# Performance work log

Hardware: AMD Instinct MI355X
Metric: run time of the kernel (lower is better)

## Reference

```python
import jax, jax.numpy as jnp
import numpy as np

TOKENS, HIDDEN, N_EXPERTS = 16384, 2048, 64
JITTER_EPS = 0.01
Z_LOSS_COEFF = 0.001


def setup_inputs() -> dict:
    key = jax.random.key(0)
    k1, k2 = jax.random.split(key)
    x = jax.random.normal(k1, (TOKENS, HIDDEN), dtype=jnp.float32)
    w = jax.random.normal(k2, (N_EXPERTS, HIDDEN), dtype=jnp.float32) * 0.02  # router weight [E,H]
    return {"x": x, "w": w}


def _route_pass(scores_sel, scores, jitter_eps):
    # scores_sel: logits possibly with -inf at already-selected expert (top-2 pass)
    # scores:     original logits (used for abs/clamp factor, as in torch code)
    mx = jnp.max(scores_sel, axis=-1, keepdims=True)                      # [N,1]
    factor = jnp.maximum(jnp.abs(scores), mx)                             # scores.abs().clamp(min=mx)
    mask = jax.lax.stop_gradient((mx - scores) / factor > 2.0 * jitter_eps)
    masked_logits = jnp.where(mask, -jnp.inf, scores_sel)
    # eval path (training=False): selected_experts = argmax of (masked-for-selection) scores
    sel = jnp.argmax(scores_sel, axis=-1)[..., None]                      # [N,1] int
    gates = jax.nn.softmax(masked_logits, axis=-1)
    # mask_for_one: selected == argmax(gates) holds deterministically in eval -> 1.0
    mult = jnp.take_along_axis(gates, sel, axis=-1)                       # [N,1]
    return mult, sel


def reference(x, w):
    logits = x @ w.T                                                      # [N,E]
    # z-loss (identity on logits in forward; scalar returned for completeness)
    z_loss = Z_LOSS_COEFF * jnp.mean(jnp.square(jax.nn.logsumexp(logits, axis=-1)))
    original_gates = jax.nn.softmax(logits, axis=-1)
    # top-1 pass
    m1, s1 = _route_pass(logits, logits, JITTER_EPS)
    # top-2 pass: mask out the first selection
    e_idx = jnp.arange(logits.shape[-1])[None, :]
    scores2 = jnp.where(e_idx == s1, -jnp.inf, logits)
    m2, s2 = _route_pass(scores2, logits, JITTER_EPS)
    multiplier = jnp.concatenate([m1, m2], axis=-1)                       # [N,2]
    selected_experts = jnp.concatenate([s1, s2], axis=-1)                 # [N,2]
    return multiplier, original_gates, selected_experts, z_loss
```

## Files before the change

### kernel.cpp

```cpp
#include <hip/hip_runtime.h>
#include <math.h>

#define TOKENS 16384
#define HIDDEN 2048
#define NEXP   64
#define MT     32
#define NBLK   (TOKENS / MT)

#define GATES_OFF (TOKENS * 2)
#define SEL_OFF   (GATES_OFF + TOKENS * NEXP)
#define Z_OFF     (SEL_OFF + TOKENS * 2)

#define WIMG_BYTES (NEXP * HIDDEN * 2 * 2)

typedef __attribute__((ext_vector_type(8))) _Float16 f16x8;
typedef __attribute__((ext_vector_type(4))) float    f32x4;

__device__ __forceinline__ float wave_sum64(float v) {
    #pragma unroll
    for (int s = 1; s < 64; s <<= 1) v += __shfl_xor(v, s, 64);
    return v;
}

__global__ __launch_bounds__(256) void wconvert(
    const float* __restrict__ w, uint4* __restrict__ wimg)
{
    const int s = blockIdx.x * 256 + threadIdx.x;
    const int c    = s >> 10;
    const int r    = s & 1023;
    const int l    = r & 63;
    const int nt   = (r >> 6) & 1;
    const int kh   = (r >> 7) & 1;
    const int term = (r >> 8) & 1;
    const int eh   = (r >> 9) & 1;
    const int e = eh * 32 + nt * 16 + (l & 15);
    const int k = c * 64 + kh * 32 + (l >> 4) * 8;

    const float* src = w + (size_t)e * HIDDEN + k;
    union { _Float16 f[8]; uint4 u; } o;
    #pragma unroll
    for (int j = 0; j < 8; ++j) {
        const float v = src[j];
        const _Float16 h = (_Float16)v;
        o.f[j] = (term == 0) ? h : (_Float16)((v - (float)h) * 4096.f);
    }
    wimg[s] = o.u;
}

__device__ __forceinline__ void cvt_split(const float4 a, const float4 b,
                                          f16x8& hi, f16x8& lo) {
    union { _Float16 f[8]; f16x8 v; } H, L;
    #pragma unroll
    for (int j = 0; j < 4; ++j) {
        const float s0 = (&a.x)[j];
        const float s1 = (&b.x)[j];
        const _Float16 h0 = (_Float16)s0;
        const _Float16 h1 = (_Float16)s1;
        H.f[j]     = h0;
        H.f[j + 4] = h1;
        L.f[j]     = (_Float16)((s0 - (float)h0) * 4096.f);
        L.f[j + 4] = (_Float16)((s1 - (float)h1) * 4096.f);
    }
    hi = H.v; lo = L.v;
}

struct Pipe {
    float4 ra0, ra1, ra2, ra3;
    f16x8  bh[4], bl[4];
};

__device__ __forceinline__ void loadA(Pipe& P, const float* ax0,
                                      const float* ax1, int s) {
    P.ra0 = *(const float4*)(ax0 + s * 32);
    P.ra1 = *(const float4*)(ax0 + s * 32 + 4);
    P.ra2 = *(const float4*)(ax1 + s * 32);
    P.ra3 = *(const float4*)(ax1 + s * 32 + 4);
}

__device__ __forceinline__ void loadB(Pipe& P, const uint4* wB, int s) {
    const uint4* p = wB + (s >> 1) * 1024 + (s & 1) * 128;
    P.bh[0] = *(const f16x8*)(p);
    P.bh[1] = *(const f16x8*)(p + 64);
    P.bh[2] = *(const f16x8*)(p + 512);
    P.bh[3] = *(const f16x8*)(p + 576);
    P.bl[0] = *(const f16x8*)(p + 256);
    P.bl[1] = *(const f16x8*)(p + 320);
    P.bl[2] = *(const f16x8*)(p + 768);
    P.bl[3] = *(const f16x8*)(p + 832);
}

__device__ __forceinline__ void domfma(const Pipe& P,
                                       const f16x8 Ah0, const f16x8 Ah1,
                                       const f16x8 Al0, const f16x8 Al1,
                                       f32x4 (&acc0)[2][4], f32x4 (&acc1)[2][4]) {
    #pragma unroll
    for (int g = 0; g < 4; ++g) {
        acc0[0][g] = __builtin_amdgcn_mfma_f32_16x16x32_f16(Ah0, P.bh[g], acc0[0][g], 0, 0, 0);
        acc1[0][g] = __builtin_amdgcn_mfma_f32_16x16x32_f16(Ah0, P.bl[g], acc1[0][g], 0, 0, 0);
        acc1[0][g] = __builtin_amdgcn_mfma_f32_16x16x32_f16(Al0, P.bh[g], acc1[0][g], 0, 0, 0);
        acc0[1][g] = __builtin_amdgcn_mfma_f32_16x16x32_f16(Ah1, P.bh[g], acc0[1][g], 0, 0, 0);
        acc1[1][g] = __builtin_amdgcn_mfma_f32_16x16x32_f16(Ah1, P.bl[g], acc1[1][g], 0, 0, 0);
        acc1[1][g] = __builtin_amdgcn_mfma_f32_16x16x32_f16(Al1, P.bh[g], acc1[1][g], 0, 0, 0);
    }
}

__global__ __launch_bounds__(256, 2) void router_main(
    const float* __restrict__ x, const uint4* __restrict__ wimg,
    float* __restrict__ out, float* __restrict__ zpartial)
{
    __shared__ __align__(16) float lg[4][32 * 66];
    __shared__ float zred[4];

    const int tid  = threadIdx.x;
    const int wv   = __builtin_amdgcn_readfirstlane(tid >> 6);
    const int lane = tid & 63;
    const int t0   = blockIdx.x * MT;

    const float* ax0 = x + (size_t)(t0 + (lane & 15)) * HIDDEN
                         + wv * 512 + (lane >> 4) * 8;
    const float* ax1 = ax0 + 16 * HIDDEN;

    const uint4* wB = wimg + wv * 8192 + lane;

    f32x4 acc0[2][4], acc1[2][4];
    #pragma unroll
    for (int mt = 0; mt < 2; ++mt)
        #pragma unroll
        for (int g = 0; g < 4; ++g) { acc0[mt][g] = (f32x4)0.f; acc1[mt][g] = (f32x4)0.f; }

    Pipe PA, PB;
    f16x8 Ah0, Ah1, Al0, Al1;

    loadA(PA, ax0, ax1, 0); loadB(PA, wB, 0);
    loadA(PB, ax0, ax1, 1); loadB(PB, wB, 1);

    #pragma unroll
    for (int s = 0; s < 16; s += 2) {
        cvt_split(PA.ra0, PA.ra1, Ah0, Al0);
        cvt_split(PA.ra2, PA.ra3, Ah1, Al1);
        if (s + 2 < 16) loadA(PA, ax0, ax1, s + 2);
        domfma(PA, Ah0, Ah1, Al0, Al1, acc0, acc1);
        if (s + 2 < 16) loadB(PA, wB, s + 2);

        cvt_split(PB.ra0, PB.ra1, Ah0, Al0);
        cvt_split(PB.ra2, PB.ra3, Ah1, Al1);
        if (s + 3 < 16) loadA(PB, ax0, ax1, s + 3);
        domfma(PB, Ah0, Ah1, Al0, Al1, acc0, acc1);
        if (s + 3 < 16) loadB(PB, wB, s + 3);
    }

    #pragma unroll
    for (int mt = 0; mt < 2; ++mt)
        #pragma unroll
        for (int g = 0; g < 4; ++g)
            #pragma unroll
            for (int r = 0; r < 4; ++r) {
                const int tok = mt * 16 + (lane >> 4) * 4 + r;
                const int e   = (g >> 1) * 32 + (g & 1) * 16 + (lane & 15);
                lg[wv][tok * 66 + e] = acc0[mt][g][r] + acc1[mt][g][r] * (1.f / 4096.f);
            }
    __syncthreads();

    float zsum = 0.f;
    for (int tt = 0; tt < 8; ++tt) {
        const int t = wv * 8 + tt;
        const int li = t * 66 + lane;
        const float v = lg[0][li] + lg[1][li] + lg[2][li] + lg[3][li];

        float bv = v; int bi = lane;
        #pragma unroll
        for (int s = 1; s < 64; s <<= 1) {
            const float ov = __shfl_xor(bv, s, 64);
            const int   oi = __shfl_xor(bi, s, 64);
            if (ov > bv || (ov == bv && oi < bi)) { bv = ov; bi = oi; }
        }
        const float max1 = bv; const int s1 = bi;

        const float e1 = expf(v - max1);
        const float sume = wave_sum64(e1);
        out[GATES_OFF + (size_t)(t0 + t) * NEXP + lane] = e1 / sume;
        const float lse = max1 + logf(sume);
        zsum += lse * lse;

        const bool mask1 = (max1 - v) > 0.02f * fmaxf(fabsf(v), max1);
        const float sum1 = wave_sum64(mask1 ? 0.f : e1);

        float bv2 = (lane == s1) ? -INFINITY : v; int bi2 = lane;
        #pragma unroll
        for (int s = 1; s < 64; s <<= 1) {
            const float ov = __shfl_xor(bv2, s, 64);
            const int   oi = __shfl_xor(bi2, s, 64);
            if (ov > bv2 || (ov == bv2 && oi < bi2)) { bv2 = ov; bi2 = oi; }
        }
        const float max2 = bv2; const int s2 = bi2;

        const bool mask2 = (max2 - v) > 0.02f * fmaxf(fabsf(v), max2);
        const float p2v = (mask2 || lane == s1) ? 0.f : expf(v - max2);
        const float sum2 = wave_sum64(p2v);

        if (lane == 0) {
            const size_t trow = (size_t)(t0 + t) * 2;
            out[trow + 0] = 1.f / sum1;
            out[trow + 1] = 1.f / sum2;
            out[SEL_OFF + trow + 0] = (float)s1;
            out[SEL_OFF + trow + 1] = (float)s2;
        }
    }

    if (lane == 0) zred[wv] = zsum;
    __syncthreads();
    if (tid == 0)
        zpartial[blockIdx.x] = zred[0] + zred[1] + zred[2] + zred[3];
}

__global__ __launch_bounds__(256) void zfinal(
    const float* __restrict__ zpartial, float* __restrict__ out)
{
    const int tid = threadIdx.x;
    float v = zpartial[tid] + zpartial[tid + 256];
    v = wave_sum64(v);
    __shared__ float red[4];
    if ((tid & 63) == 0) red[tid >> 6] = v;
    __syncthreads();
    if (tid == 0) {
        const float tot = red[0] + red[1] + red[2] + red[3];
        out[Z_OFF] = 0.001f * (tot / (float)TOKENS);
    }
}

extern "C" void kernel_launch(void* const* d_in, const int* in_sizes, int n_in,
                              void* d_out, int out_size, void* d_ws, size_t ws_size,
                              hipStream_t stream) {
    const float* x = (const float*)d_in[0];
    const float* w = (const float*)d_in[1];
    float* out = (float*)d_out;

    uint4* wimg     = (uint4*)d_ws;
    float* zpartial = (float*)((char*)d_ws + WIMG_BYTES);

    wconvert<<<128, 256, 0, stream>>>(w, wimg);
    router_main<<<NBLK, 256, 0, stream>>>(x, wimg, out, zpartial);
    zfinal<<<1, 256, 0, stream>>>(zpartial, out);
}
```

Baseline: 218.1 us.

## Fuse weight conversion and z-loss reduction into single router kernel

```diff
diff --git a/kernel.cpp b/kernel.cpp
--- a/kernel.cpp
+++ b/kernel.cpp
@@ -11,40 +11,16 @@
 #define SEL_OFF   (GATES_OFF + TOKENS * NEXP)
 #define Z_OFF     (SEL_OFF + TOKENS * 2)
 
-#define WIMG_BYTES (NEXP * HIDDEN * 2 * 2)
-
 typedef __attribute__((ext_vector_type(8))) _Float16 f16x8;
 typedef __attribute__((ext_vector_type(4))) float    f32x4;
 
+__device__ float    g_zacc = 0.f;
+__device__ unsigned g_cnt  = 0u;
+
 __device__ __forceinline__ float wave_sum64(float v) {
     #pragma unroll
     for (int s = 1; s < 64; s <<= 1) v += __shfl_xor(v, s, 64);
     return v;
-}
-
-__global__ __launch_bounds__(256) void wconvert(
-    const float* __restrict__ w, uint4* __restrict__ wimg)
-{
-    const int s = blockIdx.x * 256 + threadIdx.x;
-    const int c    = s >> 10;
-    const int r    = s & 1023;
-    const int l    = r & 63;
-    const int nt   = (r >> 6) & 1;
-    const int kh   = (r >> 7) & 1;
-    const int term = (r >> 8) & 1;
-    const int eh   = (r >> 9) & 1;
-    const int e = eh * 32 + nt * 16 + (l & 15);
-    const int k = c * 64 + kh * 32 + (l >> 4) * 8;
-
-    const float* src = w + (size_t)e * HIDDEN + k;
-    union { _Float16 f[8]; uint4 u; } o;
-    #pragma unroll
-    for (int j = 0; j < 8; ++j) {
-        const float v = src[j];
-        const _Float16 h = (_Float16)v;
-        o.f[j] = (term == 0) ? h : (_Float16)((v - (float)h) * 4096.f);
-    }
-    wimg[s] = o.u;
 }
 
 __device__ __forceinline__ void cvt_split(const float4 a, const float4 b,
@@ -64,49 +40,50 @@
     hi = H.v; lo = L.v;
 }
 
-struct Pipe {
-    float4 ra0, ra1, ra2, ra3;
-    f16x8  bh[4], bl[4];
-};
-
-__device__ __forceinline__ void loadA(Pipe& P, const float* ax0,
-                                      const float* ax1, int s) {
-    P.ra0 = *(const float4*)(ax0 + s * 32);
-    P.ra1 = *(const float4*)(ax0 + s * 32 + 4);
-    P.ra2 = *(const float4*)(ax1 + s * 32);
-    P.ra3 = *(const float4*)(ax1 + s * 32 + 4);
-}
-
-__device__ __forceinline__ void loadB(Pipe& P, const uint4* wB, int s) {
-    const uint4* p = wB + (s >> 1) * 1024 + (s & 1) * 128;
-    P.bh[0] = *(const f16x8*)(p);
-    P.bh[1] = *(const f16x8*)(p + 64);
-    P.bh[2] = *(const f16x8*)(p + 512);
-    P.bh[3] = *(const f16x8*)(p + 576);
-    P.bl[0] = *(const f16x8*)(p + 256);
-    P.bl[1] = *(const f16x8*)(p + 320);
-    P.bl[2] = *(const f16x8*)(p + 768);
-    P.bl[3] = *(const f16x8*)(p + 832);
-}
-
-__device__ __forceinline__ void domfma(const Pipe& P,
-                                       const f16x8 Ah0, const f16x8 Ah1,
-                                       const f16x8 Al0, const f16x8 Al1,
-                                       f32x4 (&acc0)[2][4], f32x4 (&acc1)[2][4]) {
+struct Stage { float4 a[4]; float4 b[8]; };
+
+__device__ __forceinline__ void load_stage(
+    Stage& S, const float* ax0, const float* ax1,
+    const float* bw0, const float* bw1, const float* bw2, const float* bw3,
+    int s)
+{
+    const int o = s * 32;
+    S.a[0] = *(const float4*)(ax0 + o);
+    S.a[1] = *(const float4*)(ax0 + o + 4);
+    S.a[2] = *(const float4*)(ax1 + o);
+    S.a[3] = *(const float4*)(ax1 + o + 4);
+    S.b[0] = *(const float4*)(bw0 + o);
+    S.b[1] = *(const float4*)(bw0 + o + 4);
+    S.b[2] = *(const float4*)(bw1 + o);
+    S.b[3] = *(const float4*)(bw1 + o + 4);
+    S.b[4] = *(const float4*)(bw2 + o);
+    S.b[5] = *(const float4*)(bw2 + o + 4);
+    S.b[6] = *(const float4*)(bw3 + o);
+    S.b[7] = *(const float4*)(bw3 + o + 4);
+}
+
+__device__ __forceinline__ void consume_stage(
+    const Stage& S, f32x4 (&acc0)[2][4], f32x4 (&acc1)[2][4])
+{
+    f16x8 Ah0, Al0, Ah1, Al1;
+    cvt_split(S.a[0], S.a[1], Ah0, Al0);
+    cvt_split(S.a[2], S.a[3], Ah1, Al1);
     #pragma unroll
     for (int g = 0; g < 4; ++g) {
-        acc0[0][g] = __builtin_amdgcn_mfma_f32_16x16x32_f16(Ah0, P.bh[g], acc0[0][g], 0, 0, 0);
-        acc1[0][g] = __builtin_amdgcn_mfma_f32_16x16x32_f16(Ah0, P.bl[g], acc1[0][g], 0, 0, 0);
-        acc1[0][g] = __builtin_amdgcn_mfma_f32_16x16x32_f16(Al0, P.bh[g], acc1[0][g], 0, 0, 0);
-        acc0[1][g] = __builtin_amdgcn_mfma_f32_16x16x32_f16(Ah1, P.bh[g], acc0[1][g], 0, 0, 0);
-        acc1[1][g] = __builtin_amdgcn_mfma_f32_16x16x32_f16(Ah1, P.bl[g], acc1[1][g], 0, 0, 0);
-        acc1[1][g] = __builtin_amdgcn_mfma_f32_16x16x32_f16(Al1, P.bh[g], acc1[1][g], 0, 0, 0);
-    }
-}
-
-__global__ __launch_bounds__(256, 2) void router_main(
-    const float* __restrict__ x, const uint4* __restrict__ wimg,
-    float* __restrict__ out, float* __restrict__ zpartial)
+        f16x8 bh, bl;
+        cvt_split(S.b[2 * g], S.b[2 * g + 1], bh, bl);
+        acc0[0][g] = __builtin_amdgcn_mfma_f32_16x16x32_f16(Ah0, bh, acc0[0][g], 0, 0, 0);
+        acc0[1][g] = __builtin_amdgcn_mfma_f32_16x16x32_f16(Ah1, bh, acc0[1][g], 0, 0, 0);
+        acc1[0][g] = __builtin_amdgcn_mfma_f32_16x16x32_f16(Ah0, bl, acc1[0][g], 0, 0, 0);
+        acc1[0][g] = __builtin_amdgcn_mfma_f32_16x16x32_f16(Al0, bh, acc1[0][g], 0, 0, 0);
+        acc1[1][g] = __builtin_amdgcn_mfma_f32_16x16x32_f16(Ah1, bl, acc1[1][g], 0, 0, 0);
+        acc1[1][g] = __builtin_amdgcn_mfma_f32_16x16x32_f16(Al1, bh, acc1[1][g], 0, 0, 0);
+    }
+}
+
+__global__ __launch_bounds__(256, 2) void router_full(
+    const float* __restrict__ x, const float* __restrict__ w,
+    float* __restrict__ out)
 {
     __shared__ __align__(16) float lg[4][32 * 66];
     __shared__ float zred[4];
@@ -116,11 +93,15 @@
     const int lane = tid & 63;
     const int t0   = blockIdx.x * MT;
 
-    const float* ax0 = x + (size_t)(t0 + (lane & 15)) * HIDDEN
-                         + wv * 512 + (lane >> 4) * 8;
+    const int kbase = wv * 512 + (lane >> 4) * 8;
+
+    const float* ax0 = x + (size_t)(t0 + (lane & 15)) * HIDDEN + kbase;
     const float* ax1 = ax0 + 16 * HIDDEN;
 
-    const uint4* wB = wimg + wv * 8192 + lane;
+    const float* bw0 = w + (size_t)(lane & 15) * HIDDEN + kbase;
+    const float* bw1 = bw0 + 16 * HIDDEN;
+    const float* bw2 = bw0 + 32 * HIDDEN;
+    const float* bw3 = bw0 + 48 * HIDDEN;
 
     f32x4 acc0[2][4], acc1[2][4];
     #pragma unroll
@@ -128,25 +109,17 @@
         #pragma unroll
         for (int g = 0; g < 4; ++g) { acc0[mt][g] = (f32x4)0.f; acc1[mt][g] = (f32x4)0.f; }
 
-    Pipe PA, PB;
-    f16x8 Ah0, Ah1, Al0, Al1;
-
-    loadA(PA, ax0, ax1, 0); loadB(PA, wB, 0);
-    loadA(PB, ax0, ax1, 1); loadB(PB, wB, 1);
+    Stage SA, SB;
+
+    load_stage(SA, ax0, ax1, bw0, bw1, bw2, bw3, 0);
+    load_stage(SB, ax0, ax1, bw0, bw1, bw2, bw3, 1);
 
     #pragma unroll
     for (int s = 0; s < 16; s += 2) {
-        cvt_split(PA.ra0, PA.ra1, Ah0, Al0);
-        cvt_split(PA.ra2, PA.ra3, Ah1, Al1);
-        if (s + 2 < 16) loadA(PA, ax0, ax1, s + 2);
-        domfma(PA, Ah0, Ah1, Al0, Al1, acc0, acc1);
-        if (s + 2 < 16) loadB(PA, wB, s + 2);
-
-        cvt_split(PB.ra0, PB.ra1, Ah0, Al0);
-        cvt_split(PB.ra2, PB.ra3, Ah1, Al1);
-        if (s + 3 < 16) loadA(PB, ax0, ax1, s + 3);
-        domfma(PB, Ah0, Ah1, Al0, Al1, acc0, acc1);
-        if (s + 3 < 16) loadB(PB, wB, s + 3);
+        consume_stage(SA, acc0, acc1);
+        if (s + 2 < 16) load_stage(SA, ax0, ax1, bw0, bw1, bw2, bw3, s + 2);
+        consume_stage(SB, acc0, acc1);
+        if (s + 3 < 16) load_stage(SB, ax0, ax1, bw0, bw1, bw2, bw3, s + 3);
     }
 
     #pragma unroll
@@ -156,7 +129,7 @@
             #pragma unroll
             for (int r = 0; r < 4; ++r) {
                 const int tok = mt * 16 + (lane >> 4) * 4 + r;
-                const int e   = (g >> 1) * 32 + (g & 1) * 16 + (lane & 15);
+                const int e   = g * 16 + (lane & 15);
                 lg[wv][tok * 66 + e] = acc0[mt][g][r] + acc1[mt][g][r] * (1.f / 4096.f);
             }
     __syncthreads();
@@ -209,22 +182,18 @@
 
     if (lane == 0) zred[wv] = zsum;
     __syncthreads();
-    if (tid == 0)
-        zpartial[blockIdx.x] = zred[0] + zred[1] + zred[2] + zred[3];
-}
-
-__global__ __launch_bounds__(256) void zfinal(
-    const float* __restrict__ zpartial, float* __restrict__ out)
-{
-    const int tid = threadIdx.x;
-    float v = zpartial[tid] + zpartial[tid + 256];
-    v = wave_sum64(v);
-    __shared__ float red[4];
-    if ((tid & 63) == 0) red[tid >> 6] = v;
-    __syncthreads();
+
     if (tid == 0) {
-        const float tot = red[0] + red[1] + red[2] + red[3];
-        out[Z_OFF] = 0.001f * (tot / (float)TOKENS);
+        const float bz = zred[0] + zred[1] + zred[2] + zred[3];
+        atomicAdd(&g_zacc, bz);
+        __threadfence();
+        const unsigned old = atomicAdd(&g_cnt, 1u);
+        if (old == NBLK - 1) {
+            __threadfence();
+            const float tot = atomicExch(&g_zacc, 0.f);
+            atomicExch(&g_cnt, 0u);
+            out[Z_OFF] = 0.001f * (tot / (float)TOKENS);
+        }
     }
 }
 
@@ -234,11 +203,7 @@
     const float* x = (const float*)d_in[0];
     const float* w = (const float*)d_in[1];
     float* out = (float*)d_out;
-
-    uint4* wimg     = (uint4*)d_ws;
-    float* zpartial = (float*)((char*)d_ws + WIMG_BYTES);
-
-    wconvert<<<128, 256, 0, stream>>>(w, wimg);
-    router_main<<<NBLK, 256, 0, stream>>>(x, wimg, out, zpartial);
-    zfinal<<<1, 256, 0, stream>>>(zpartial, out);
-}
+    (void)d_ws; (void)ws_size;
+
+    router_full<<<NBLK, 256, 0, stream>>>(x, w, out);
+}
```

Measured after the change: 238.6 us. 1.09x slower.

## Halve token tile per block, raise occupancy, fuse z-loss reduction via atomics

Applied to the files above, without the earlier changes.

```diff
diff --git a/kernel.cpp b/kernel.cpp
--- a/kernel.cpp
+++ b/kernel.cpp
@@ -4,7 +4,7 @@
 #define TOKENS 16384
 #define HIDDEN 2048
 #define NEXP   64
-#define MT     32
+#define MT     16
 #define NBLK   (TOKENS / MT)
 
 #define GATES_OFF (TOKENS * 2)
@@ -15,6 +15,9 @@
 
 typedef __attribute__((ext_vector_type(8))) _Float16 f16x8;
 typedef __attribute__((ext_vector_type(4))) float    f32x4;
+
+__device__ float    g_zacc = 0.f;
+__device__ unsigned g_cnt  = 0u;
 
 __device__ __forceinline__ float wave_sum64(float v) {
     #pragma unroll
@@ -64,51 +67,44 @@
     hi = H.v; lo = L.v;
 }
 
-struct Pipe {
-    float4 ra0, ra1, ra2, ra3;
+struct Stage {
+    float4 a0, a1;
     f16x8  bh[4], bl[4];
 };
 
-__device__ __forceinline__ void loadA(Pipe& P, const float* ax0,
-                                      const float* ax1, int s) {
-    P.ra0 = *(const float4*)(ax0 + s * 32);
-    P.ra1 = *(const float4*)(ax0 + s * 32 + 4);
-    P.ra2 = *(const float4*)(ax1 + s * 32);
-    P.ra3 = *(const float4*)(ax1 + s * 32 + 4);
-}
-
-__device__ __forceinline__ void loadB(Pipe& P, const uint4* wB, int s) {
+__device__ __forceinline__ void load_stage(Stage& S, const float* ax0,
+                                           const uint4* wB, int s) {
+    S.a0 = *(const float4*)(ax0 + s * 32);
+    S.a1 = *(const float4*)(ax0 + s * 32 + 4);
     const uint4* p = wB + (s >> 1) * 1024 + (s & 1) * 128;
-    P.bh[0] = *(const f16x8*)(p);
-    P.bh[1] = *(const f16x8*)(p + 64);
-    P.bh[2] = *(const f16x8*)(p + 512);
-    P.bh[3] = *(const f16x8*)(p + 576);
-    P.bl[0] = *(const f16x8*)(p + 256);
-    P.bl[1] = *(const f16x8*)(p + 320);
-    P.bl[2] = *(const f16x8*)(p + 768);
-    P.bl[3] = *(const f16x8*)(p + 832);
-}
-
-__device__ __forceinline__ void domfma(const Pipe& P,
-                                       const f16x8 Ah0, const f16x8 Ah1,
-                                       const f16x8 Al0, const f16x8 Al1,
-                                       f32x4 (&acc0)[2][4], f32x4 (&acc1)[2][4]) {
+    S.bh[0] = *(const f16x8*)(p);
+    S.bh[1] = *(const f16x8*)(p + 64);
+    S.bh[2] = *(const f16x8*)(p + 512);
+    S.bh[3] = *(const f16x8*)(p + 576);
+    S.bl[0] = *(const f16x8*)(p + 256);
+    S.bl[1] = *(const f16x8*)(p + 320);
+    S.bl[2] = *(const f16x8*)(p + 768);
+    S.bl[3] = *(const f16x8*)(p + 832);
+}
+
+__device__ __forceinline__ void consume_stage(
+    const Stage& S, f32x4 (&acc0)[4], f32x4 (&acc1)[4])
+{
+    f16x8 Ah, Al;
+    cvt_split(S.a0, S.a1, Ah, Al);
     #pragma unroll
     for (int g = 0; g < 4; ++g) {
-        acc0[0][g] = __builtin_amdgcn_mfma_f32_16x16x32_f16(Ah0, P.bh[g], acc0[0][g], 0, 0, 0);
-        acc1[0][g] = __builtin_amdgcn_mfma_f32_16x16x32_f16(Ah0, P.bl[g], acc1[0][g], 0, 0, 0);
-        acc1[0][g] = __builtin_amdgcn_mfma_f32_16x16x32_f16(Al0, P.bh[g], acc1[0][g], 0, 0, 0);
-        acc0[1][g] = __builtin_amdgcn_mfma_f32_16x16x32_f16(Ah1, P.bh[g], acc0[1][g], 0, 0, 0);
-        acc1[1][g] = __builtin_amdgcn_mfma_f32_16x16x32_f16(Ah1, P.bl[g], acc1[1][g], 0, 0, 0);
-        acc1[1][g] = __builtin_amdgcn_mfma_f32_16x16x32_f16(Al1, P.bh[g], acc1[1][g], 0, 0, 0);
-    }
-}
-
-__global__ __launch_bounds__(256, 2) void router_main(
+        acc0[g] = __builtin_amdgcn_mfma_f32_16x16x32_f16(Ah, S.bh[g], acc0[g], 0, 0, 0);
+        acc1[g] = __builtin_amdgcn_mfma_f32_16x16x32_f16(Ah, S.bl[g], acc1[g], 0, 0, 0);
+        acc1[g] = __builtin_amdgcn_mfma_f32_16x16x32_f16(Al, S.bh[g], acc1[g], 0, 0, 0);
+    }
+}
+
+__global__ __launch_bounds__(256, 3) void router_main(
     const float* __restrict__ x, const uint4* __restrict__ wimg,
-    float* __restrict__ out, float* __restrict__ zpartial)
+    float* __restrict__ out)
 {
-    __shared__ __align__(16) float lg[4][32 * 66];
+    __shared__ __align__(16) float lg[4][MT * 66];
     __shared__ float zred[4];
 
     const int tid  = threadIdx.x;
@@ -118,52 +114,38 @@
 
     const float* ax0 = x + (size_t)(t0 + (lane & 15)) * HIDDEN
                          + wv * 512 + (lane >> 4) * 8;
-    const float* ax1 = ax0 + 16 * HIDDEN;
 
     const uint4* wB = wimg + wv * 8192 + lane;
 
-    f32x4 acc0[2][4], acc1[2][4];
-    #pragma unroll
-    for (int mt = 0; mt < 2; ++mt)
+    f32x4 acc0[4], acc1[4];
+    #pragma unroll
+    for (int g = 0; g < 4; ++g) { acc0[g] = (f32x4)0.f; acc1[g] = (f32x4)0.f; }
+
+    Stage SA, SB;
+    load_stage(SA, ax0, wB, 0);
+    load_stage(SB, ax0, wB, 1);
+
+    #pragma unroll
+    for (int s = 0; s < 16; s += 2) {
+        consume_stage(SA, acc0, acc1);
+        if (s + 2 < 16) load_stage(SA, ax0, wB, s + 2);
+        consume_stage(SB, acc0, acc1);
+        if (s + 3 < 16) load_stage(SB, ax0, wB, s + 3);
+    }
+
+    #pragma unroll
+    for (int g = 0; g < 4; ++g)
         #pragma unroll
-        for (int g = 0; g < 4; ++g) { acc0[mt][g] = (f32x4)0.f; acc1[mt][g] = (f32x4)0.f; }
-
-    Pipe PA, PB;
-    f16x8 Ah0, Ah1, Al0, Al1;
-
-    loadA(PA, ax0, ax1, 0); loadB(PA, wB, 0);
-    loadA(PB, ax0, ax1, 1); loadB(PB, wB, 1);
-
-    #pragma unroll
-    for (int s = 0; s < 16; s += 2) {
-        cvt_split(PA.ra0, PA.ra1, Ah0, Al0);
-        cvt_split(PA.ra2, PA.ra3, Ah1, Al1);
-        if (s + 2 < 16) loadA(PA, ax0, ax1, s + 2);
-        domfma(PA, Ah0, Ah1, Al0, Al1, acc0, acc1);
-        if (s + 2 < 16) loadB(PA, wB, s + 2);
-
-        cvt_split(PB.ra0, PB.ra1, Ah0, Al0);
-        cvt_split(PB.ra2, PB.ra3, Ah1, Al1);
-        if (s + 3 < 16) loadA(PB, ax0, ax1, s + 3);
-        domfma(PB, Ah0, Ah1, Al0, Al1, acc0, acc1);
-        if (s + 3 < 16) loadB(PB, wB, s + 3);
-    }
-
-    #pragma unroll
-    for (int mt = 0; mt < 2; ++mt)
-        #pragma unroll
-        for (int g = 0; g < 4; ++g)
-            #pragma unroll
-            for (int r = 0; r < 4; ++r) {
-                const int tok = mt * 16 + (lane >> 4) * 4 + r;
-                const int e   = (g >> 1) * 32 + (g & 1) * 16 + (lane & 15);
-                lg[wv][tok * 66 + e] = acc0[mt][g][r] + acc1[mt][g][r] * (1.f / 4096.f);
-            }
+        for (int r = 0; r < 4; ++r) {
+            const int tok = (lane >> 4) * 4 + r;
+            const int e   = (g >> 1) * 32 + (g & 1) * 16 + (lane & 15);
+            lg[wv][tok * 66 + e] = acc0[g][r] + acc1[g][r] * (1.f / 4096.f);
+        }
     __syncthreads();
 
     float zsum = 0.f;
-    for (int tt = 0; tt < 8; ++tt) {
-        const int t = wv * 8 + tt;
+    for (int tt = 0; tt < 4; ++tt) {
+        const int t = wv * 4 + tt;
         const int li = t * 66 + lane;
         const float v = lg[0][li] + lg[1][li] + lg[2][li] + lg[3][li];
 
@@ -209,22 +191,18 @@
 
     if (lane == 0) zred[wv] = zsum;
     __syncthreads();
-    if (tid == 0)
-        zpartial[blockIdx.x] = zred[0] + zred[1] + zred[2] + zred[3];
-}
-
-__global__ __launch_bounds__(256) void zfinal(
-    const float* __restrict__ zpartial, float* __restrict__ out)
-{
-    const int tid = threadIdx.x;
-    float v = zpartial[tid] + zpartial[tid + 256];
-    v = wave_sum64(v);
-    __shared__ float red[4];
-    if ((tid & 63) == 0) red[tid >> 6] = v;
-    __syncthreads();
+
     if (tid == 0) {
-        const float tot = red[0] + red[1] + red[2] + red[3];
-        out[Z_OFF] = 0.001f * (tot / (float)TOKENS);
+        const float bz = zred[0] + zred[1] + zred[2] + zred[3];
+        atomicAdd(&g_zacc, bz);
+        __threadfence();
+        const unsigned old = atomicAdd(&g_cnt, 1u);
+        if (old == NBLK - 1) {
+            __threadfence();
+            const float tot = atomicExch(&g_zacc, 0.f);
+            atomicExch(&g_cnt, 0u);
+            out[Z_OFF] = 0.001f * (tot / (float)TOKENS);
+        }
     }
 }
 
@@ -235,10 +213,8 @@
     const float* w = (const float*)d_in[1];
     float* out = (float*)d_out;
 
-    uint4* wimg     = (uint4*)d_ws;
-    float* zpartial = (float*)((char*)d_ws + WIMG_BYTES);
+    uint4* wimg = (uint4*)d_ws;
 
     wconvert<<<128, 256, 0, stream>>>(w, wimg);
-    router_main<<<NBLK, 256, 0, stream>>>(x, wimg, out, zpartial);
-    zfinal<<<1, 256, 0, stream>>>(zpartial, out);
-}
+    router_main<<<NBLK, 256, 0, stream>>>(x, wimg, out);
+}
```

Result: slower. 241.5 us (+10.7%).
